# Performance work log

Hardware: AMD Instinct MI355X
Metric: run time of the kernel (lower is better)

## Reference

```python
import jax, jax.numpy as jnp
import numpy as np

B, L, D = 2, 2048, 2048
HQ, HKV = 32, 8
HD = D // HQ            # 64
G = HQ // HKV           # 4


def setup_inputs() -> dict:
    key = jax.random.key(0)
    ks = jax.random.split(key, 9)
    s = 1.0 / np.sqrt(D)
    return {
        "x": jax.random.normal(ks[0], (B, L, D), jnp.float32),
        "Wq": jax.random.normal(ks[1], (D, HQ * HD), jnp.float32) * s,
        "bq": jnp.zeros((HQ * HD,), jnp.float32),
        "Wk": jax.random.normal(ks[2], (D, HKV * HD), jnp.float32) * s,
        "bk": jnp.zeros((HKV * HD,), jnp.float32),
        "Wv": jax.random.normal(ks[3], (D, HKV * HD), jnp.float32) * s,
        "bv": jnp.zeros((HKV * HD,), jnp.float32),
        "Wo": jax.random.normal(ks[4], (HQ * HD, D), jnp.float32) * s,
        "bo": jnp.zeros((D,), jnp.float32),
    }


def reference(x, Wq, bq, Wk, bk, Wv, bv, Wo, bo):
    # projections
    q = x @ Wq + bq                                   # [B, L, HQ*HD]
    k = x @ Wk + bk                                   # [B, L, HKV*HD]
    v = x @ Wv + bv
    # split heads; group q heads by kv head: [B, HKV, G, L, HD]
    q = q.reshape(B, L, HKV, G, HD).transpose(0, 2, 3, 1, 4)
    k = k.reshape(B, L, HKV, HD).transpose(0, 2, 1, 3)   # [B, HKV, L, HD]
    v = v.reshape(B, L, HKV, HD).transpose(0, 2, 1, 3)
    scale = 1.0 / np.sqrt(HD)
    # scores [B, HKV, G, Lq, Lk] -- same math as repeat_kv + matmul
    scores = jnp.einsum('bhgqd,bhkd->bhgqk', q, k) * scale
    attn = jax.nn.softmax(scores, axis=-1)
    ctx = jnp.einsum('bhgqk,bhkd->bhgqd', attn, v)       # [B, HKV, G, L, HD]
    # merge heads back to [B, L, HQ*HD]
    ctx = ctx.transpose(0, 3, 1, 2, 4).reshape(B, L, HQ * HD)
    return ctx @ Wo + bo
```

## Files before the change

### kernel.cpp

```cpp
#include <hip/hip_runtime.h>
#include <cstdint>
#include <cstring>


#define L_SEQ 2048
#define D_MODEL 2048
#define M_ROWS 4096
#define KV_COLS 512
#define ATTN_SCALE 0.18033688011112042f

typedef __bf16 bf16x8 __attribute__((ext_vector_type(8)));
typedef float f32x4 __attribute__((ext_vector_type(4)));
typedef float f32x16 __attribute__((ext_vector_type(16)));

__device__ __forceinline__ f32x4 zero4() {
    f32x4 v; v[0] = 0.f; v[1] = 0.f; v[2] = 0.f; v[3] = 0.f; return v;
}

__device__ __forceinline__ unsigned short f2bf(float x) {
    unsigned u = __builtin_bit_cast(unsigned, x);
    u = (u + 0x7FFFu + ((u >> 16) & 1u)) >> 16;
    return (unsigned short)u;
}

__device__ __forceinline__ unsigned pk_bf16(float a, float b) {
#if __has_builtin(__builtin_amdgcn_cvt_pk_bf16_f32)
    typedef __bf16 bf16x2 __attribute__((ext_vector_type(2)));
    bf16x2 r = __builtin_amdgcn_cvt_pk_bf16_f32(a, b);
    return __builtin_bit_cast(unsigned, r);
#else
    return (unsigned)f2bf(a) | ((unsigned)f2bf(b) << 16);
#endif
}

__device__ __forceinline__ f32x4 mfma16(uint4 a, uint4 b, f32x4 c) {
    return __builtin_amdgcn_mfma_f32_16x16x32_bf16(
        __builtin_bit_cast(bf16x8, a), __builtin_bit_cast(bf16x8, b), c, 0, 0, 0);
}
__device__ __forceinline__ f32x16 mfma32(uint4 a, uint4 b, f32x16 c) {
    return __builtin_amdgcn_mfma_f32_32x32x16_bf16(
        __builtin_bit_cast(bf16x8, a), __builtin_bit_cast(bf16x8, b), c, 0, 0, 0);
}

__device__ __forceinline__ void gl_lds16(const unsigned short* g, unsigned short* l) {
    __builtin_amdgcn_global_load_lds(
        (const __attribute__((address_space(1))) unsigned int*)g,
        (__attribute__((address_space(3))) unsigned int*)l, 16, 0, 0);
}

#if __has_builtin(__builtin_amdgcn_exp2f)
#define EXP2F(x) __builtin_amdgcn_exp2f(x)
#else
#define EXP2F(x) exp2f(x)
#endif


__global__ __launch_bounds__(256) void cast_x_kernel(const float* __restrict__ in,
                                                     unsigned short* __restrict__ out,
                                                     int n4) {
    int i = blockIdx.x * 256 + threadIdx.x;
    if (i >= n4) return;
    float4 v = ((const float4*)in)[i];
    uint2 o;
    o.x = pk_bf16(v.x, v.y);
    o.y = pk_bf16(v.z, v.w);
    ((uint2*)out)[i] = o;
}

__global__ __launch_bounds__(256) void transpose_cast_kernel(const float* __restrict__ in,
                                                             unsigned short* __restrict__ out,
                                                             int N, int row_off) {
    __shared__ float tile[32][33];
    const int n0 = blockIdx.x * 32, k0 = blockIdx.y * 32;
    const int tc = threadIdx.x & 31, tr = threadIdx.x >> 5;
#pragma unroll
    for (int i = 0; i < 4; ++i)
        tile[tr + i * 8][tc] = in[(size_t)(k0 + tr + i * 8) * N + n0 + tc];
    __syncthreads();
#pragma unroll
    for (int i = 0; i < 4; ++i)
        out[(size_t)(row_off + n0 + tr + i * 8) * 2048 + k0 + tc] = f2bf(tile[tc][tr + i * 8]);
}


__device__ __forceinline__ void gemm_core_2048(const unsigned short* __restrict__ A,
                                               const unsigned short* __restrict__ Bt,
                                               int m_block, int n_block,
                                               unsigned short* smA, unsigned short* smB,
                                               f32x4 acc[4][4]) {
    const int tid = threadIdx.x;
    const int w = tid >> 6, lane = tid & 63;
    const int wm = w >> 1, wn = w & 1;
    const int lr = lane & 15, lg = lane >> 4;

#pragma unroll
    for (int i = 0; i < 4; ++i)
#pragma unroll
        for (int j = 0; j < 4; ++j) acc[i][j] = zero4();

    const int rowA = m_block * 128 + w * 32 + (lane >> 2);
    const int rowB = n_block * 128 + w * 32 + (lane >> 2);
    const int kcol = (lane & 3) * 8;
    const unsigned short* gA0 = A + (size_t)rowA * 2048 + kcol;
    const unsigned short* gA1 = gA0 + (size_t)16 * 2048;
    const unsigned short* gB0 = Bt + (size_t)rowB * 2048 + kcol;
    const unsigned short* gB1 = gB0 + (size_t)16 * 2048;
    unsigned short* lA0 = smA + (w * 32) * 32;
    unsigned short* lA1 = smA + (w * 32 + 16) * 32;
    unsigned short* lB0 = smB + (w * 32) * 32;
    unsigned short* lB1 = smB + (w * 32 + 16) * 32;

    for (int kt = 0; kt < 64; ++kt) {
        gl_lds16(gA0 + kt * 32, lA0);
        gl_lds16(gA1 + kt * 32, lA1);
        gl_lds16(gB0 + kt * 32, lB0);
        gl_lds16(gB1 + kt * 32, lB1);
        __syncthreads();
        uint4 af[4], bfg[4];
#pragma unroll
        for (int i = 0; i < 4; ++i)
            af[i] = *(const uint4*)(smA + (wm * 64 + i * 16 + lr) * 32 + lg * 8);
#pragma unroll
        for (int j = 0; j < 4; ++j)
            bfg[j] = *(const uint4*)(smB + (wn * 64 + j * 16 + lr) * 32 + lg * 8);
#pragma unroll
        for (int i = 0; i < 4; ++i)
#pragma unroll
            for (int j = 0; j < 4; ++j)
                acc[i][j] = mfma16(af[i], bfg[j], acc[i][j]);
        __syncthreads();
    }
}

__global__ __launch_bounds__(256) void gemm_qkv_kernel(
    const unsigned short* __restrict__ Xb, const unsigned short* __restrict__ Wt,
    const float* __restrict__ bq, const float* __restrict__ bk, const float* __restrict__ bv,
    unsigned short* __restrict__ Qb, unsigned short* __restrict__ Kb,
    unsigned short* __restrict__ Vb) {
    __shared__ __align__(16) unsigned short smA[128 * 32];
    __shared__ __align__(16) unsigned short smB[128 * 32];
    f32x4 acc[4][4];
    gemm_core_2048(Xb, Wt, blockIdx.x, blockIdx.y, smA, smB, acc);

    const int tid = threadIdx.x;
    const int w = tid >> 6, lane = tid & 63;
    const int wm = w >> 1, wn = w & 1;
    const int lr = lane & 15, lg = lane >> 4;
    const int nbase = blockIdx.y * 128;

    unsigned short* outp; int ldo, noff; const float* bias; float scale;
    if (nbase < 2048)      { outp = Qb; ldo = 2048; noff = 0;    bias = bq; scale = 1.f; }
    else if (nbase < 2560) { outp = Kb; ldo = 512;  noff = 2048; bias = bk; scale = ATTN_SCALE; }
    else                   { outp = Vb; ldo = 512;  noff = 2560; bias = bv; scale = 1.f; }

#pragma unroll
    for (int i = 0; i < 4; ++i) {
        const int mrow = blockIdx.x * 128 + wm * 64 + i * 16 + lg * 4;
#pragma unroll
        for (int j = 0; j < 4; ++j) {
            const int nloc = nbase + wn * 64 + j * 16 + lr - noff;
            const float bb = bias[nloc];
#pragma unroll
            for (int r = 0; r < 4; ++r)
                outp[(size_t)(mrow + r) * ldo + nloc] = f2bf((acc[i][j][r] + bb) * scale);
        }
    }
}

__global__ __launch_bounds__(256) void gemm_out_kernel(
    const unsigned short* __restrict__ Cb, const unsigned short* __restrict__ Wot,
    const float* __restrict__ bo, float* __restrict__ out) {
    __shared__ __align__(16) unsigned short smA[128 * 32];
    __shared__ __align__(16) unsigned short smB[128 * 32];
    f32x4 acc[4][4];
    gemm_core_2048(Cb, Wot, blockIdx.x, blockIdx.y, smA, smB, acc);

    const int tid = threadIdx.x;
    const int w = tid >> 6, lane = tid & 63;
    const int wm = w >> 1, wn = w & 1;
    const int lr = lane & 15, lg = lane >> 4;

#pragma unroll
    for (int i = 0; i < 4; ++i) {
        const int mrow = blockIdx.x * 128 + wm * 64 + i * 16 + lg * 4;
#pragma unroll
        for (int j = 0; j < 4; ++j) {
            const int ncol = blockIdx.y * 128 + wn * 64 + j * 16 + lr;
            const float bb = bo[ncol];
#pragma unroll
            for (int r = 0; r < 4; ++r)
                out[(size_t)(mrow + r) * 2048 + ncol] = acc[i][j][r] + bb;
        }
    }
}


__global__ __launch_bounds__(256, 4) void attn_kernel(const unsigned short* __restrict__ Qb,
                                                      const unsigned short* __restrict__ Kb,
                                                      const unsigned short* __restrict__ Vb,
                                                      unsigned short* __restrict__ ctx) {
    __shared__ __align__(16) unsigned short ks[128 * 64];
    __shared__ __align__(16) unsigned short vt[64 * 136];

    const int qt = blockIdx.x, hq = blockIdx.y, b = blockIdx.z;
    const int kvh = hq >> 2;
    const int tid = threadIdx.x;
    const int w = tid >> 6, lane = tid & 63;
    const int l31 = lane & 31, h = lane >> 5;

    const int qrow = b * L_SEQ + qt * 128 + w * 32 + l31;
    const unsigned short* qp = Qb + (size_t)qrow * 2048 + hq * 64;
    uint4 qf[4];
#pragma unroll
    for (int dh = 0; dh < 4; ++dh) qf[dh] = *(const uint4*)(qp + dh * 16 + h * 8);

    f32x16 o0, o1;
#pragma unroll
    for (int r = 0; r < 16; ++r) { o0[r] = 0.f; o1[r] = 0.f; }
    float l_acc = 0.f;

    const size_t kvbase = (size_t)(b * L_SEQ) * KV_COLS + kvh * 64;

    for (int t = 0; t < L_SEQ / 128; ++t) {
        const int k0 = t * 128;
#pragma unroll
        for (int s = 0; s < 4; ++s) {
            const int blk = w * 4 + s;
            const int r = blk * 8 + (lane >> 3);
            const int cch = (lane & 7) ^ (r & 7);
            gl_lds16(Kb + kvbase + (size_t)(k0 + r) * KV_COLS + cch * 8, ks + blk * 512);
        }
        unsigned* vtu = (unsigned*)vt;
#pragma unroll
        for (int it = 0; it < 2; ++it) {
            const int rp = lane;
            const int dg = it * 4 + w;
            const unsigned short* vsrc = Vb + kvbase + (size_t)(k0 + 2 * rp) * KV_COLS + dg * 8;
            union { uint4 v; unsigned short s[8]; } ua, ub;
            ua.v = *(const uint4*)vsrc;
            ub.v = *(const uint4*)(vsrc + KV_COLS);
#pragma unroll
            for (int j = 0; j < 8; ++j)
                vtu[(dg * 8 + j) * 68 + rp] = (unsigned)ua.s[j] | ((unsigned)ub.s[j] << 16);
        }
        __syncthreads();

#pragma unroll
        for (int c = 0; c < 4; ++c) {
            f32x16 s;
#pragma unroll
            for (int r = 0; r < 16; ++r) s[r] = 0.f;
#pragma unroll
            for (int dh = 0; dh < 4; ++dh) {
                uint4 kf = *(const uint4*)&ks[(c * 32 + l31) * 64 +
                                              (((dh * 2 + h) ^ (l31 & 7)) * 8)];
                s = mfma32(kf, qf[dh], s);
            }
            unsigned E[4][2];
            float lsum = 0.f;
#pragma unroll
            for (int g = 0; g < 4; ++g) {
                float e0 = EXP2F(s[4 * g + 0]);
                float e1 = EXP2F(s[4 * g + 1]);
                float e2 = EXP2F(s[4 * g + 2]);
                float e3 = EXP2F(s[4 * g + 3]);
                lsum += (e0 + e1) + (e2 + e3);
                E[g][0] = pk_bf16(e0, e1);
                E[g][1] = pk_bf16(e2, e3);
            }
            l_acc += lsum;
#pragma unroll
            for (int tau = 0; tau < 2; ++tau) {
                unsigned pub0 = h ? E[2 * tau][0] : E[2 * tau + 1][0];
                unsigned pub1 = h ? E[2 * tau][1] : E[2 * tau + 1][1];
                unsigned R0 = (unsigned)__shfl_xor((int)pub0, 32, 64);
                unsigned R1 = (unsigned)__shfl_xor((int)pub1, 32, 64);
                uint4 pf;
                pf.x = h ? R0 : E[2 * tau][0];
                pf.y = h ? R1 : E[2 * tau][1];
                pf.z = h ? E[2 * tau + 1][0] : R0;
                pf.w = h ? E[2 * tau + 1][1] : R1;
                const int kcol = c * 32 + tau * 16 + h * 8;
                uint4 vf0 = *(const uint4*)&vt[(0 * 32 + l31) * 136 + kcol];
                uint4 vf1 = *(const uint4*)&vt[(1 * 32 + l31) * 136 + kcol];
                o0 = mfma32(vf0, pf, o0);
                o1 = mfma32(vf1, pf, o1);
            }
        }
        __syncthreads();
    }

    float l_tot = l_acc + __shfl_xor(l_acc, 32, 64);
    const float rl = 1.f / l_tot;
    __syncthreads();
    unsigned* ep = (unsigned*)vt + w * 1088;
#pragma unroll
    for (int dt = 0; dt < 2; ++dt) {
        const f32x16& o = dt ? o1 : o0;
#pragma unroll
        for (int g = 0; g < 4; ++g)
#pragma unroll
            for (int p = 0; p < 2; ++p) {
                const int dv = dt * 16 + 4 * g + 2 * h + p;
                ep[l31 * 34 + dv] = pk_bf16(o[4 * g + 2 * p] * rl, o[4 * g + 2 * p + 1] * rl);
            }
    }
    __builtin_amdgcn_s_waitcnt(0);
#pragma unroll
    for (int p = 0; p < 4; ++p) {
        const int qr = (lane >> 3) + p * 8;
        const int cch = lane & 7;
        uint4 vv = *(const uint4*)((const unsigned short*)ep + qr * 68 + cch * 8);
        *(uint4*)(ctx + (size_t)(b * L_SEQ + qt * 128 + w * 32 + qr) * 2048 +
                  hq * 64 + cch * 8) = vv;
    }
}


extern "C" void kernel_launch(void* const* d_in, const int* in_sizes, int n_in,
                              void* d_out, int out_size, void* d_ws, size_t ws_size,
                              hipStream_t stream) {
    const float* x  = (const float*)d_in[0];
    const float* Wq = (const float*)d_in[1];
    const float* bq = (const float*)d_in[2];
    const float* Wk = (const float*)d_in[3];
    const float* bk = (const float*)d_in[4];
    const float* Wv = (const float*)d_in[5];
    const float* bv = (const float*)d_in[6];
    const float* Wo = (const float*)d_in[7];
    const float* bo = (const float*)d_in[8];
    float* out = (float*)d_out;

    char* ws = (char*)d_ws;
    size_t off = 0;
    auto alloc = [&](size_t bytes) {
        char* p = ws + off;
        off += (bytes + 255) & ~(size_t)255;
        return p;
    };
    unsigned short* Wqkvt = (unsigned short*)alloc((size_t)3072 * 2048 * 2);
    unsigned short* Wot   = (unsigned short*)alloc((size_t)2048 * 2048 * 2);
    unsigned short* Xb    = (unsigned short*)alloc((size_t)M_ROWS * 2048 * 2);
    unsigned short* Qb    = (unsigned short*)alloc((size_t)M_ROWS * 2048 * 2);
    unsigned short* Kb    = (unsigned short*)alloc((size_t)M_ROWS * KV_COLS * 2);
    unsigned short* Vb    = (unsigned short*)alloc((size_t)M_ROWS * KV_COLS * 2);
    unsigned short* Cb    = Xb;

    cast_x_kernel<<<(M_ROWS * 2048 / 4 + 255) / 256, 256, 0, stream>>>(x, Xb,
                                                                       M_ROWS * 2048 / 4);
    transpose_cast_kernel<<<dim3(64, 64), 256, 0, stream>>>(Wq, Wqkvt, 2048, 0);
    transpose_cast_kernel<<<dim3(16, 64), 256, 0, stream>>>(Wk, Wqkvt, 512, 2048);
    transpose_cast_kernel<<<dim3(16, 64), 256, 0, stream>>>(Wv, Wqkvt, 512, 2560);
    transpose_cast_kernel<<<dim3(64, 64), 256, 0, stream>>>(Wo, Wot, 2048, 0);
    gemm_qkv_kernel<<<dim3(32, 24), 256, 0, stream>>>(Xb, Wqkvt, bq, bk, bv, Qb, Kb, Vb);
    attn_kernel<<<dim3(16, 32, 2), 256, 0, stream>>>(Qb, Kb, Vb, Cb);
    gemm_out_kernel<<<dim3(32, 16), 256, 0, stream>>>(Cb, Wot, bo, out);
}
```

Baseline: 383.0 us.

## Split attention over key halves, pre-transpose V in QKV GEMM, add merge

The QKV GEMM epilogue now writes V already transposed per kv-head (d-major), so the attention kernel can load V tiles with async global-to-LDS copies instead of a register transpose. Attention is split into two key-range halves (doubling the grid), uses smaller 64-key tiles with less LDS and higher occupancy hints, and writes unnormalized partial outputs plus row sums. A new merge kernel adds the two partials and normalizes. This relies on there being no running max, so partials can simply be added. The cost is extra bf16 partial traffic, rounding of the partials, and one more launch.

```diff
diff --git a/kernel.cpp b/kernel.cpp
--- a/kernel.cpp
+++ b/kernel.cpp
@@ -21,6 +21,10 @@
     unsigned u = __builtin_bit_cast(unsigned, x);
     u = (u + 0x7FFFu + ((u >> 16) & 1u)) >> 16;
     return (unsigned short)u;
+}
+__device__ __forceinline__ float bf2fs(unsigned short h) {
+    unsigned u = ((unsigned)h) << 16;
+    return __builtin_bit_cast(float, u);
 }
 
 __device__ __forceinline__ unsigned pk_bf16(float a, float b) {
@@ -136,7 +140,7 @@
     const unsigned short* __restrict__ Xb, const unsigned short* __restrict__ Wt,
     const float* __restrict__ bq, const float* __restrict__ bk, const float* __restrict__ bv,
     unsigned short* __restrict__ Qb, unsigned short* __restrict__ Kb,
-    unsigned short* __restrict__ Vb) {
+    unsigned short* __restrict__ Vt) {
     __shared__ __align__(16) unsigned short smA[128 * 32];
     __shared__ __align__(16) unsigned short smB[128 * 32];
     f32x4 acc[4][4];
@@ -148,10 +152,28 @@
     const int lr = lane & 15, lg = lane >> 4;
     const int nbase = blockIdx.y * 128;
 
+    if (nbase >= 2560) {
+#pragma unroll
+        for (int i = 0; i < 4; ++i) {
+            const int mrow = blockIdx.x * 128 + wm * 64 + i * 16 + lg * 4;
+            const int b = mrow >> 11, l = mrow & 2047;
+#pragma unroll
+            for (int j = 0; j < 4; ++j) {
+                const int nloc = nbase + wn * 64 + j * 16 + lr - 2560;
+                const int kvh = nloc >> 6, d = nloc & 63;
+                const float bb = bv[nloc];
+                uint2 pv;
+                pv.x = pk_bf16(acc[i][j][0] + bb, acc[i][j][1] + bb);
+                pv.y = pk_bf16(acc[i][j][2] + bb, acc[i][j][3] + bb);
+                *(uint2*)(Vt + ((size_t)((b * 8 + kvh) * 64 + d)) * 2048 + l) = pv;
+            }
+        }
+        return;
+    }
+
     unsigned short* outp; int ldo, noff; const float* bias; float scale;
     if (nbase < 2048)      { outp = Qb; ldo = 2048; noff = 0;    bias = bq; scale = 1.f; }
-    else if (nbase < 2560) { outp = Kb; ldo = 512;  noff = 2048; bias = bk; scale = ATTN_SCALE; }
-    else                   { outp = Vb; ldo = 512;  noff = 2560; bias = bv; scale = 1.f; }
+    else                   { outp = Kb; ldo = 512;  noff = 2048; bias = bk; scale = ATTN_SCALE; }
 
 #pragma unroll
     for (int i = 0; i < 4; ++i) {
@@ -195,14 +217,17 @@
 }
 
 
-__global__ __launch_bounds__(256, 4) void attn_kernel(const unsigned short* __restrict__ Qb,
-                                                      const unsigned short* __restrict__ Kb,
-                                                      const unsigned short* __restrict__ Vb,
-                                                      unsigned short* __restrict__ ctx) {
-    __shared__ __align__(16) unsigned short ks[128 * 64];
-    __shared__ __align__(16) unsigned short vt[64 * 136];
-
-    const int qt = blockIdx.x, hq = blockIdx.y, b = blockIdx.z;
+__global__ __launch_bounds__(256, 6) void attn_kernel(
+    const unsigned short* __restrict__ Qb, const unsigned short* __restrict__ Kb,
+    const unsigned short* __restrict__ Vtg,
+    unsigned short* __restrict__ Po0, unsigned short* __restrict__ Po1,
+    float* __restrict__ Ls) {
+    __shared__ __align__(16) unsigned short smem[8704];
+    unsigned short* ks = smem;
+    unsigned short* vt = smem + 4096;
+
+    const int qt = blockIdx.x, hq = blockIdx.y;
+    const int b = blockIdx.z >> 1, half = blockIdx.z & 1;
     const int kvh = hq >> 2;
     const int tid = threadIdx.x;
     const int w = tid >> 6, lane = tid & 63;
@@ -219,34 +244,24 @@
     for (int r = 0; r < 16; ++r) { o0[r] = 0.f; o1[r] = 0.f; }
     float l_acc = 0.f;
 
-    const size_t kvbase = (size_t)(b * L_SEQ) * KV_COLS + kvh * 64;
-
-    for (int t = 0; t < L_SEQ / 128; ++t) {
-        const int k0 = t * 128;
-#pragma unroll
-        for (int s = 0; s < 4; ++s) {
-            const int blk = w * 4 + s;
-            const int r = blk * 8 + (lane >> 3);
-            const int cch = (lane & 7) ^ (r & 7);
-            gl_lds16(Kb + kvbase + (size_t)(k0 + r) * KV_COLS + cch * 8, ks + blk * 512);
-        }
-        unsigned* vtu = (unsigned*)vt;
-#pragma unroll
-        for (int it = 0; it < 2; ++it) {
-            const int rp = lane;
-            const int dg = it * 4 + w;
-            const unsigned short* vsrc = Vb + kvbase + (size_t)(k0 + 2 * rp) * KV_COLS + dg * 8;
-            union { uint4 v; unsigned short s[8]; } ua, ub;
-            ua.v = *(const uint4*)vsrc;
-            ub.v = *(const uint4*)(vsrc + KV_COLS);
-#pragma unroll
-            for (int j = 0; j < 8; ++j)
-                vtu[(dg * 8 + j) * 68 + rp] = (unsigned)ua.s[j] | ((unsigned)ub.s[j] << 16);
+    const size_t kbase = (size_t)(b * L_SEQ) * KV_COLS + kvh * 64;
+    const size_t vbase = (size_t)((b * 8 + kvh) * 64) * 2048;
+    const int rr = lane >> 3;
+    const int swl = (lane & 7) ^ rr;
+
+    for (int t = 0; t < 16; ++t) {
+        const int k0 = half * 1024 + t * 64;
+#pragma unroll
+        for (int s2 = 0; s2 < 2; ++s2) {
+            const int blk = w * 2 + s2;
+            const int row = blk * 8 + rr;
+            gl_lds16(Kb + kbase + (size_t)(k0 + row) * KV_COLS + swl * 8, ks + blk * 512);
+            gl_lds16(Vtg + vbase + (size_t)row * 2048 + k0 + swl * 8, vt + blk * 512);
         }
         __syncthreads();
 
 #pragma unroll
-        for (int c = 0; c < 4; ++c) {
+        for (int c = 0; c < 2; ++c) {
             f32x16 s;
 #pragma unroll
             for (int r = 0; r < 16; ++r) s[r] = 0.f;
@@ -280,9 +295,9 @@
                 pf.y = h ? R1 : E[2 * tau][1];
                 pf.z = h ? E[2 * tau + 1][0] : R0;
                 pf.w = h ? E[2 * tau + 1][1] : R1;
-                const int kcol = c * 32 + tau * 16 + h * 8;
-                uint4 vf0 = *(const uint4*)&vt[(0 * 32 + l31) * 136 + kcol];
-                uint4 vf1 = *(const uint4*)&vt[(1 * 32 + l31) * 136 + kcol];
+                const int ch = ((c * 4 + tau * 2 + h) ^ (l31 & 7)) * 8;
+                uint4 vf0 = *(const uint4*)&vt[(size_t)l31 * 64 + ch];
+                uint4 vf1 = *(const uint4*)&vt[(size_t)(32 + l31) * 64 + ch];
                 o0 = mfma32(vf0, pf, o0);
                 o1 = mfma32(vf1, pf, o1);
             }
@@ -291,9 +306,12 @@
     }
 
     float l_tot = l_acc + __shfl_xor(l_acc, 32, 64);
-    const float rl = 1.f / l_tot;
+    if (h == 0)
+        Ls[(size_t)half * (M_ROWS * 32) + (size_t)qrow * 32 + hq] = l_tot;
+
     __syncthreads();
-    unsigned* ep = (unsigned*)vt + w * 1088;
+    unsigned short* po = half ? Po1 : Po0;
+    unsigned* ep = (unsigned*)smem + w * 1088;
 #pragma unroll
     for (int dt = 0; dt < 2; ++dt) {
         const f32x16& o = dt ? o1 : o0;
@@ -302,7 +320,7 @@
 #pragma unroll
             for (int p = 0; p < 2; ++p) {
                 const int dv = dt * 16 + 4 * g + 2 * h + p;
-                ep[l31 * 34 + dv] = pk_bf16(o[4 * g + 2 * p] * rl, o[4 * g + 2 * p + 1] * rl);
+                ep[l31 * 34 + dv] = pk_bf16(o[4 * g + 2 * p], o[4 * g + 2 * p + 1]);
             }
     }
     __builtin_amdgcn_s_waitcnt(0);
@@ -311,9 +329,36 @@
         const int qr = (lane >> 3) + p * 8;
         const int cch = lane & 7;
         uint4 vv = *(const uint4*)((const unsigned short*)ep + qr * 68 + cch * 8);
-        *(uint4*)(ctx + (size_t)(b * L_SEQ + qt * 128 + w * 32 + qr) * 2048 +
+        *(uint4*)(po + (size_t)(b * L_SEQ + qt * 128 + w * 32 + qr) * 2048 +
                   hq * 64 + cch * 8) = vv;
     }
+}
+
+
+__global__ __launch_bounds__(256) void merge_kernel(
+    const unsigned short* __restrict__ Po0, const unsigned short* __restrict__ Po1,
+    const float* __restrict__ Ls, unsigned short* __restrict__ ctx) {
+    const int gid = blockIdx.x * 256 + threadIdx.x;
+    const int row = gid >> 8, c8 = gid & 255;
+    const int hq = c8 >> 3;
+    const float l = Ls[(size_t)row * 32 + hq] + Ls[(size_t)(M_ROWS * 32) + (size_t)row * 32 + hq];
+    const float rl = 1.f / l;
+    const uint4 a = ((const uint4*)(Po0 + (size_t)row * 2048))[c8];
+    const uint4 bq4 = ((const uint4*)(Po1 + (size_t)row * 2048))[c8];
+    const unsigned ua[4] = {a.x, a.y, a.z, a.w};
+    const unsigned ub[4] = {bq4.x, bq4.y, bq4.z, bq4.w};
+    uint4 res;
+    unsigned rr[4];
+#pragma unroll
+    for (int k = 0; k < 4; ++k) {
+        const float lo = bf2fs((unsigned short)(ua[k] & 0xffff)) +
+                         bf2fs((unsigned short)(ub[k] & 0xffff));
+        const float hi = bf2fs((unsigned short)(ua[k] >> 16)) +
+                         bf2fs((unsigned short)(ub[k] >> 16));
+        rr[k] = pk_bf16(lo * rl, hi * rl);
+    }
+    res.x = rr[0]; res.y = rr[1]; res.z = rr[2]; res.w = rr[3];
+    *(uint4*)(ctx + (size_t)row * 2048 + c8 * 8) = res;
 }
 
 
@@ -343,8 +388,11 @@
     unsigned short* Xb    = (unsigned short*)alloc((size_t)M_ROWS * 2048 * 2);
     unsigned short* Qb    = (unsigned short*)alloc((size_t)M_ROWS * 2048 * 2);
     unsigned short* Kb    = (unsigned short*)alloc((size_t)M_ROWS * KV_COLS * 2);
-    unsigned short* Vb    = (unsigned short*)alloc((size_t)M_ROWS * KV_COLS * 2);
-    unsigned short* Cb    = Xb;
+    unsigned short* Vt    = (unsigned short*)alloc((size_t)M_ROWS * KV_COLS * 2);
+    unsigned short* Po1   = (unsigned short*)alloc((size_t)M_ROWS * 2048 * 2);
+    float*          Ls    = (float*)alloc((size_t)2 * M_ROWS * 32 * 4);
+    unsigned short* Po0   = Xb;
+    unsigned short* Cb    = Qb;
 
     cast_x_kernel<<<(M_ROWS * 2048 / 4 + 255) / 256, 256, 0, stream>>>(x, Xb,
                                                                        M_ROWS * 2048 / 4);
@@ -352,7 +400,8 @@
     transpose_cast_kernel<<<dim3(16, 64), 256, 0, stream>>>(Wk, Wqkvt, 512, 2048);
     transpose_cast_kernel<<<dim3(16, 64), 256, 0, stream>>>(Wv, Wqkvt, 512, 2560);
     transpose_cast_kernel<<<dim3(64, 64), 256, 0, stream>>>(Wo, Wot, 2048, 0);
-    gemm_qkv_kernel<<<dim3(32, 24), 256, 0, stream>>>(Xb, Wqkvt, bq, bk, bv, Qb, Kb, Vb);
-    attn_kernel<<<dim3(16, 32, 2), 256, 0, stream>>>(Qb, Kb, Vb, Cb);
+    gemm_qkv_kernel<<<dim3(32, 24), 256, 0, stream>>>(Xb, Wqkvt, bq, bk, bv, Qb, Kb, Vt);
+    attn_kernel<<<dim3(16, 32, 4), 256, 0, stream>>>(Qb, Kb, Vt, Po0, Po1, Ls);
+    merge_kernel<<<M_ROWS * 2048 / 8 / 256, 256, 0, stream>>>(Po0, Po1, Ls, Cb);
     gemm_out_kernel<<<dim3(32, 16), 256, 0, stream>>>(Cb, Wot, bo, out);
 }
```

After: 425.2 us. +11.0%, slower.

## Pre-transpose V globally and process two query tiles per wave in attention

Applied to the files above, without the earlier changes.

Adds a separate kernel that writes V transposed to global memory, so the attention kernel can load V tiles with async global-to-LDS copies using an XOR swizzle instead of per-thread transposing scatter stores. Each wave now handles 64 query rows (two 32-row tiles), which reuses each K and V LDS fragment for twice as many MFMAs and halves the grid. The cost is more accumulator registers (launch bounds lowered to 2 blocks per CU), an extra transpose kernel launch, and an extra V-sized workspace buffer.

```diff
diff --git a/kernel.cpp b/kernel.cpp
--- a/kernel.cpp
+++ b/kernel.cpp
@@ -80,6 +80,20 @@
 #pragma unroll
     for (int i = 0; i < 4; ++i)
         out[(size_t)(row_off + n0 + tr + i * 8) * 2048 + k0 + tc] = f2bf(tile[tc][tr + i * 8]);
+}
+
+__global__ __launch_bounds__(256) void transpose_v_kernel(const unsigned short* __restrict__ Vb,
+                                                          unsigned short* __restrict__ Vt) {
+    __shared__ unsigned short tile[32][33];
+    const int c0 = blockIdx.x * 32, l0 = blockIdx.y * 32, b = blockIdx.z;
+    const int tc = threadIdx.x & 31, tr = threadIdx.x >> 5;
+#pragma unroll
+    for (int i = 0; i < 4; ++i)
+        tile[tr + i * 8][tc] = Vb[(size_t)(b * 2048 + l0 + tr + i * 8) * KV_COLS + c0 + tc];
+    __syncthreads();
+#pragma unroll
+    for (int i = 0; i < 4; ++i)
+        Vt[(size_t)(b * 512 + c0 + tr + i * 8) * 2048 + l0 + tc] = tile[tc][tr + i * 8];
 }
 
 
@@ -195,12 +209,13 @@
 }
 
 
-__global__ __launch_bounds__(256, 4) void attn_kernel(const unsigned short* __restrict__ Qb,
+__global__ __launch_bounds__(256, 2) void attn_kernel(const unsigned short* __restrict__ Qb,
                                                       const unsigned short* __restrict__ Kb,
-                                                      const unsigned short* __restrict__ Vb,
+                                                      const unsigned short* __restrict__ Vtg,
                                                       unsigned short* __restrict__ ctx) {
-    __shared__ __align__(16) unsigned short ks[128 * 64];
-    __shared__ __align__(16) unsigned short vt[64 * 136];
+    __shared__ __align__(16) unsigned short smem[16384];
+    unsigned short* ks = smem;
+    unsigned short* vt = smem + 8192;
 
     const int qt = blockIdx.x, hq = blockIdx.y, b = blockIdx.z;
     const int kvh = hq >> 2;
@@ -208,111 +223,137 @@
     const int w = tid >> 6, lane = tid & 63;
     const int l31 = lane & 31, h = lane >> 5;
 
-    const int qrow = b * L_SEQ + qt * 128 + w * 32 + l31;
-    const unsigned short* qp = Qb + (size_t)qrow * 2048 + hq * 64;
-    uint4 qf[4];
-#pragma unroll
-    for (int dh = 0; dh < 4; ++dh) qf[dh] = *(const uint4*)(qp + dh * 16 + h * 8);
-
-    f32x16 o0, o1;
-#pragma unroll
-    for (int r = 0; r < 16; ++r) { o0[r] = 0.f; o1[r] = 0.f; }
-    float l_acc = 0.f;
-
-    const size_t kvbase = (size_t)(b * L_SEQ) * KV_COLS + kvh * 64;
-
-    for (int t = 0; t < L_SEQ / 128; ++t) {
+    const int qbase = qt * 256 + w * 64;
+    uint4 qf[2][4];
+#pragma unroll
+    for (int u = 0; u < 2; ++u) {
+        const unsigned short* qp =
+            Qb + (size_t)(b * L_SEQ + qbase + u * 32 + l31) * 2048 + hq * 64;
+#pragma unroll
+        for (int dh = 0; dh < 4; ++dh)
+            qf[u][dh] = *(const uint4*)(qp + dh * 16 + h * 8);
+    }
+
+    f32x16 o00, o01, o10, o11;
+#pragma unroll
+    for (int r = 0; r < 16; ++r) { o00[r] = 0.f; o01[r] = 0.f; o10[r] = 0.f; o11[r] = 0.f; }
+    float l_acc0 = 0.f, l_acc1 = 0.f;
+
+    const size_t kbase = (size_t)(b * L_SEQ) * KV_COLS + kvh * 64;
+    const size_t vbase = (size_t)((b * 8 + kvh) * 64) * 2048;
+
+    const int rrk = lane >> 3, cpk = lane & 7;
+    const int drv = lane >> 4, cpv = lane & 15;
+
+    for (int t = 0; t < 16; ++t) {
         const int k0 = t * 128;
 #pragma unroll
         for (int s = 0; s < 4; ++s) {
-            const int blk = w * 4 + s;
-            const int r = blk * 8 + (lane >> 3);
-            const int cch = (lane & 7) ^ (r & 7);
-            gl_lds16(Kb + kvbase + (size_t)(k0 + r) * KV_COLS + cch * 8, ks + blk * 512);
-        }
-        unsigned* vtu = (unsigned*)vt;
-#pragma unroll
-        for (int it = 0; it < 2; ++it) {
-            const int rp = lane;
-            const int dg = it * 4 + w;
-            const unsigned short* vsrc = Vb + kvbase + (size_t)(k0 + 2 * rp) * KV_COLS + dg * 8;
-            union { uint4 v; unsigned short s[8]; } ua, ub;
-            ua.v = *(const uint4*)vsrc;
-            ub.v = *(const uint4*)(vsrc + KV_COLS);
-#pragma unroll
-            for (int j = 0; j < 8; ++j)
-                vtu[(dg * 8 + j) * 68 + rp] = (unsigned)ua.s[j] | ((unsigned)ub.s[j] << 16);
+            const int blkk = w * 4 + s;
+            gl_lds16(Kb + kbase + (size_t)(k0 + blkk * 8 + rrk) * KV_COLS + ((cpk ^ rrk) * 8),
+                     ks + blkk * 512);
+            const int blkv = w * 4 + s;
+            const int d = blkv * 4 + drv;
+            gl_lds16(Vtg + vbase + (size_t)d * 2048 + k0 + ((cpv ^ (d & 15)) * 8),
+                     vt + blkv * 512);
         }
         __syncthreads();
 
 #pragma unroll
         for (int c = 0; c < 4; ++c) {
-            f32x16 s;
-#pragma unroll
-            for (int r = 0; r < 16; ++r) s[r] = 0.f;
-#pragma unroll
-            for (int dh = 0; dh < 4; ++dh) {
-                uint4 kf = *(const uint4*)&ks[(c * 32 + l31) * 64 +
-                                              (((dh * 2 + h) ^ (l31 & 7)) * 8)];
-                s = mfma32(kf, qf[dh], s);
+            uint4 kf[4];
+#pragma unroll
+            for (int dh = 0; dh < 4; ++dh)
+                kf[dh] = *(const uint4*)&ks[(c * 32 + l31) * 64 +
+                                            (((dh * 2 + h) ^ (l31 & 7)) * 8)];
+            unsigned E0[4][2], E1[4][2];
+#pragma unroll
+            for (int u = 0; u < 2; ++u) {
+                f32x16 s;
+#pragma unroll
+                for (int r = 0; r < 16; ++r) s[r] = 0.f;
+#pragma unroll
+                for (int dh = 0; dh < 4; ++dh) s = mfma32(kf[dh], qf[u][dh], s);
+                float lsum = 0.f;
+#pragma unroll
+                for (int g = 0; g < 4; ++g) {
+                    float e0 = EXP2F(s[4 * g + 0]);
+                    float e1 = EXP2F(s[4 * g + 1]);
+                    float e2 = EXP2F(s[4 * g + 2]);
+                    float e3 = EXP2F(s[4 * g + 3]);
+                    lsum += (e0 + e1) + (e2 + e3);
+                    if (u == 0) { E0[g][0] = pk_bf16(e0, e1); E0[g][1] = pk_bf16(e2, e3); }
+                    else        { E1[g][0] = pk_bf16(e0, e1); E1[g][1] = pk_bf16(e2, e3); }
+                }
+                if (u == 0) l_acc0 += lsum; else l_acc1 += lsum;
             }
-            unsigned E[4][2];
-            float lsum = 0.f;
-#pragma unroll
-            for (int g = 0; g < 4; ++g) {
-                float e0 = EXP2F(s[4 * g + 0]);
-                float e1 = EXP2F(s[4 * g + 1]);
-                float e2 = EXP2F(s[4 * g + 2]);
-                float e3 = EXP2F(s[4 * g + 3]);
-                lsum += (e0 + e1) + (e2 + e3);
-                E[g][0] = pk_bf16(e0, e1);
-                E[g][1] = pk_bf16(e2, e3);
+            const int posv = (c * 4) ^ (l31 & 15);
+#pragma unroll
+            for (int tau = 0; tau < 2; ++tau) {
+                const int pos = ((c * 4 + tau * 2 + h) ^ (l31 & 15)) * 8;
+                uint4 vf0 = *(const uint4*)&vt[(size_t)l31 * 128 + pos];
+                uint4 vf1 = *(const uint4*)&vt[(size_t)(32 + l31) * 128 + pos];
+                {
+                    unsigned pub0 = h ? E0[2 * tau][0] : E0[2 * tau + 1][0];
+                    unsigned pub1 = h ? E0[2 * tau][1] : E0[2 * tau + 1][1];
+                    unsigned R0 = (unsigned)__shfl_xor((int)pub0, 32, 64);
+                    unsigned R1 = (unsigned)__shfl_xor((int)pub1, 32, 64);
+                    uint4 pf;
+                    pf.x = h ? R0 : E0[2 * tau][0];
+                    pf.y = h ? R1 : E0[2 * tau][1];
+                    pf.z = h ? E0[2 * tau + 1][0] : R0;
+                    pf.w = h ? E0[2 * tau + 1][1] : R1;
+                    o00 = mfma32(vf0, pf, o00);
+                    o01 = mfma32(vf1, pf, o01);
+                }
+                {
+                    unsigned pub0 = h ? E1[2 * tau][0] : E1[2 * tau + 1][0];
+                    unsigned pub1 = h ? E1[2 * tau][1] : E1[2 * tau + 1][1];
+                    unsigned R0 = (unsigned)__shfl_xor((int)pub0, 32, 64);
+                    unsigned R1 = (unsigned)__shfl_xor((int)pub1, 32, 64);
+                    uint4 pf;
+                    pf.x = h ? R0 : E1[2 * tau][0];
+                    pf.y = h ? R1 : E1[2 * tau][1];
+                    pf.z = h ? E1[2 * tau + 1][0] : R0;
+                    pf.w = h ? E1[2 * tau + 1][1] : R1;
+                    o10 = mfma32(vf0, pf, o10);
+                    o11 = mfma32(vf1, pf, o11);
+                }
             }
-            l_acc += lsum;
-#pragma unroll
-            for (int tau = 0; tau < 2; ++tau) {
-                unsigned pub0 = h ? E[2 * tau][0] : E[2 * tau + 1][0];
-                unsigned pub1 = h ? E[2 * tau][1] : E[2 * tau + 1][1];
-                unsigned R0 = (unsigned)__shfl_xor((int)pub0, 32, 64);
-                unsigned R1 = (unsigned)__shfl_xor((int)pub1, 32, 64);
-                uint4 pf;
-                pf.x = h ? R0 : E[2 * tau][0];
-                pf.y = h ? R1 : E[2 * tau][1];
-                pf.z = h ? E[2 * tau + 1][0] : R0;
-                pf.w = h ? E[2 * tau + 1][1] : R1;
-                const int kcol = c * 32 + tau * 16 + h * 8;
-                uint4 vf0 = *(const uint4*)&vt[(0 * 32 + l31) * 136 + kcol];
-                uint4 vf1 = *(const uint4*)&vt[(1 * 32 + l31) * 136 + kcol];
-                o0 = mfma32(vf0, pf, o0);
-                o1 = mfma32(vf1, pf, o1);
-            }
+            (void)posv;
         }
         __syncthreads();
     }
 
-    float l_tot = l_acc + __shfl_xor(l_acc, 32, 64);
-    const float rl = 1.f / l_tot;
     __syncthreads();
-    unsigned* ep = (unsigned*)vt + w * 1088;
-#pragma unroll
-    for (int dt = 0; dt < 2; ++dt) {
-        const f32x16& o = dt ? o1 : o0;
-#pragma unroll
-        for (int g = 0; g < 4; ++g)
-#pragma unroll
-            for (int p = 0; p < 2; ++p) {
-                const int dv = dt * 16 + 4 * g + 2 * h + p;
-                ep[l31 * 34 + dv] = pk_bf16(o[4 * g + 2 * p] * rl, o[4 * g + 2 * p + 1] * rl);
-            }
-    }
-    __builtin_amdgcn_s_waitcnt(0);
-#pragma unroll
-    for (int p = 0; p < 4; ++p) {
-        const int qr = (lane >> 3) + p * 8;
-        const int cch = lane & 7;
-        uint4 vv = *(const uint4*)((const unsigned short*)ep + qr * 68 + cch * 8);
-        *(uint4*)(ctx + (size_t)(b * L_SEQ + qt * 128 + w * 32 + qr) * 2048 +
-                  hq * 64 + cch * 8) = vv;
+    unsigned* ep = (unsigned*)smem + w * 1088;
+#pragma unroll
+    for (int u = 0; u < 2; ++u) {
+        const float la = u ? l_acc1 : l_acc0;
+        const float l_tot = la + __shfl_xor(la, 32, 64);
+        const float rl = 1.f / l_tot;
+#pragma unroll
+        for (int dt = 0; dt < 2; ++dt) {
+            const f32x16& o = u ? (dt ? o11 : o10) : (dt ? o01 : o00);
+#pragma unroll
+            for (int g = 0; g < 4; ++g)
+#pragma unroll
+                for (int p = 0; p < 2; ++p) {
+                    const int dv = dt * 16 + 4 * g + 2 * h + p;
+                    ep[l31 * 34 + dv] =
+                        pk_bf16(o[4 * g + 2 * p] * rl, o[4 * g + 2 * p + 1] * rl);
+                }
+        }
+        __builtin_amdgcn_s_waitcnt(0);
+#pragma unroll
+        for (int p = 0; p < 4; ++p) {
+            const int qr = (lane >> 3) + p * 8;
+            const int cch = lane & 7;
+            uint4 vv = *(const uint4*)((const unsigned short*)ep + qr * 68 + cch * 8);
+            *(uint4*)(ctx + (size_t)(b * L_SEQ + qbase + u * 32 + qr) * 2048 +
+                      hq * 64 + cch * 8) = vv;
+        }
+        __builtin_amdgcn_s_waitcnt(0);
     }
 }
 
@@ -344,6 +385,7 @@
     unsigned short* Qb    = (unsigned short*)alloc((size_t)M_ROWS * 2048 * 2);
     unsigned short* Kb    = (unsigned short*)alloc((size_t)M_ROWS * KV_COLS * 2);
     unsigned short* Vb    = (unsigned short*)alloc((size_t)M_ROWS * KV_COLS * 2);
+    unsigned short* Vt    = (unsigned short*)alloc((size_t)M_ROWS * KV_COLS * 2);
     unsigned short* Cb    = Xb;
 
     cast_x_kernel<<<(M_ROWS * 2048 / 4 + 255) / 256, 256, 0, stream>>>(x, Xb,
@@ -353,6 +395,7 @@
     transpose_cast_kernel<<<dim3(16, 64), 256, 0, stream>>>(Wv, Wqkvt, 512, 2560);
     transpose_cast_kernel<<<dim3(64, 64), 256, 0, stream>>>(Wo, Wot, 2048, 0);
     gemm_qkv_kernel<<<dim3(32, 24), 256, 0, stream>>>(Xb, Wqkvt, bq, bk, bv, Qb, Kb, Vb);
-    attn_kernel<<<dim3(16, 32, 2), 256, 0, stream>>>(Qb, Kb, Vb, Cb);
+    transpose_v_kernel<<<dim3(16, 64, 2), 256, 0, stream>>>(Vb, Vt);
+    attn_kernel<<<dim3(8, 32, 2), 256, 0, stream>>>(Qb, Kb, Vt, Cb);
     gemm_out_kernel<<<dim3(32, 16), 256, 0, stream>>>(Cb, Wot, bo, out);
 }
```

After: 347.7 us. 1.1x faster.
